# Kernel tuning notes

Hardware: AMD Instinct MI355X
Metric: run time of the kernel (lower is better)

The kernel has to match this reference:

```python
import jax, jax.numpy as jnp
import numpy as np

VOCAB = 90000
MAX_ID = 95000
EFFECT_DIM = 758
ADD_DIM = 10
EMBED_DIM = 768  # EFFECT_DIM + ADD_DIM
CTX = 1024
MAX_SYN = 8


def setup_inputs() -> dict:
    key = jax.random.key(0)
    k_ids, k_emb, k_rev, k_tab, k_msk = jax.random.split(key, 5)
    ids = jax.random.randint(k_ids, (CTX,), 0, VOCAB, dtype=jnp.int64)
    W_emb = jax.random.normal(k_emb, (MAX_ID, EFFECT_DIM), dtype=jnp.float32)
    W_rev = jax.random.normal(k_rev, (EMBED_DIM, MAX_ID), dtype=jnp.float32)
    padding = 0.1 * jnp.ones((CTX, ADD_DIM), dtype=jnp.float32)
    # synonym ids live in [VOCAB, MAX_ID); only some slots are active (variable-length lists)
    syn_table = jax.random.randint(k_tab, (MAX_ID, MAX_SYN), VOCAB, MAX_ID, dtype=jnp.int32)
    syn_mask = jax.random.randint(k_msk, (MAX_ID, MAX_SYN), 0, 2, dtype=jnp.int32)
    # tokens >= VOCAB (synonym ids themselves) have no synonyms
    syn_mask = syn_mask.at[VOCAB:].set(0)
    return {"ids": ids, "W_emb": W_emb, "W_rev": W_rev, "padding": padding,
            "syn_table": syn_table, "syn_mask": syn_mask}


def reference(ids, W_emb, W_rev, padding, syn_table, syn_mask):
    # VirtualEmbedding: base gather + masked synonym gather/scale/accumulate.
    # i_sum is computed BEFORE the synonym loop in the original, so each
    # synonym contribution is independent -> vectorized masked reduction.
    # (Dropout in eval mode is the identity.)
    base = W_emb[ids]                              # [L, D]
    syn_ids = syn_table[ids]                       # [L, K]
    syn = W_emb[syn_ids]                           # [L, K, D]
    mask = syn_mask[ids].astype(base.dtype)        # [L, K]
    i_sum = jnp.sum(base, axis=-1, keepdims=True)  # [L, 1]
    s_sum = jnp.sum(syn, axis=-1)                  # [L, K]
    d = i_sum / s_sum                              # [L, K]
    emb = base + jnp.einsum('lk,lkd->ld', mask * d, syn)
    # concat fixed context padding, then ReverseEmbedding projection to vocab
    full = jnp.concatenate([emb, padding], axis=1)  # [L, EMBED_DIM]
    return full @ W_rev                             # [L, MAX_ID]
```

## Files before the change

kernel.cpp:

```cpp
#include <hip/hip_runtime.h>
#include <stdint.h>

#define EFFECT_DIM 758
#define ADD_DIM 10
#define EMBED_DIM 768
#define NCOLS 95000
#define NSYN 8
#define NROWS 1024
#define NT256 372
#define TILE_B 32768

typedef __attribute__((ext_vector_type(8))) __bf16 bf16x8;
typedef __attribute__((ext_vector_type(16))) float f32x16;
typedef __attribute__((ext_vector_type(4))) uint32_t u32x4;


static __device__ __forceinline__ uint32_t pack2(float a, float b) {
  uint32_t r;
  asm("v_cvt_pk_bf16_f32 %0, %1, %2" : "=v"(r) : "v"(a), "v"(b));
  return r;
}

#define GLOAD16(src, dst)                                                   \
  __builtin_amdgcn_global_load_lds(                                         \
      (const __attribute__((address_space(1))) uint32_t*)(src),             \
      (__attribute__((address_space(3))) uint32_t*)(dst), 16, 0, 0)

#define F4C(f, i) ((i) == 0 ? (f).x : (i) == 1 ? (f).y : (i) == 2 ? (f).z : (f).w)

__global__ __launch_bounds__(256) void emb_kernel(
    const int* __restrict__ ids, const float* __restrict__ W_emb,
    const float* __restrict__ padding, const int* __restrict__ syn_table,
    const int* __restrict__ syn_mask, char* __restrict__ ws)
{
  const int l = blockIdx.x;
  const int t = threadIdx.x;
  const int id = ids[l];
  int sid[NSYN];
  int msk[NSYN];
#pragma unroll
  for (int k = 0; k < NSYN; ++k) {
    sid[k] = syn_table[id * NSYN + k];
    msk[k] = syn_mask[id * NSYN + k];
  }

  double p[9] = {0, 0, 0, 0, 0, 0, 0, 0, 0};
  for (int d = t; d < EFFECT_DIM; d += 256) {
    p[0] += (double)W_emb[(size_t)id * EFFECT_DIM + d];
#pragma unroll
    for (int k = 0; k < NSYN; ++k)
      p[k + 1] += (double)W_emb[(size_t)sid[k] * EFFECT_DIM + d];
  }

  __shared__ double s_red[9][4];
  const int w = t >> 6;
#pragma unroll
  for (int k = 0; k < 9; ++k) {
    double v = p[k];
#pragma unroll
    for (int off = 32; off > 0; off >>= 1) v += __shfl_down(v, off, 64);
    if ((t & 63) == 0) s_red[k][w] = v;
  }
  __syncthreads();

  const double isum = s_red[0][0] + s_red[0][1] + s_red[0][2] + s_red[0][3];
  float coef[NSYN];
#pragma unroll
  for (int k = 0; k < NSYN; ++k) {
    double ss = s_red[k + 1][0] + s_red[k + 1][1] + s_red[k + 1][2] + s_red[k + 1][3];
    coef[k] = msk[k] ? (float)(isum / ss) : 0.0f;
  }

  const int r = l & 255;
  char* wbase = ws + (size_t)(l >> 8) * (12 * TILE_B);

  for (int j = t; j < 384; j += 256) {
    const int d0 = 2 * j;
    float v0, v1;
    if (d0 < EFFECT_DIM) {
      const float* bp = W_emb + (size_t)id * EFFECT_DIM + d0;
      v0 = bp[0];
      v1 = bp[1];
#pragma unroll
      for (int k = 0; k < NSYN; ++k) {
        const float* sp = W_emb + (size_t)sid[k] * EFFECT_DIM + d0;
        v0 = fmaf(coef[k], sp[0], v0);
        v1 = fmaf(coef[k], sp[1], v1);
      }
    } else {
      v0 = padding[l * ADD_DIM + (d0 - EFFECT_DIM)];
      v1 = padding[l * ADD_DIM + (d0 + 1 - EFFECT_DIM)];
    }
    const int ks   = j >> 5;
    const int jl   = j & 31;
    const int kk   = jl >> 3;
    const int byte = (jl & 7) * 4;
    const int lane = (r & 31) + ((byte >> 4) << 5);
    *(uint32_t*)(wbase + ks * TILE_B + kk * 8192 + (r >> 5) * 1024 +
                 lane * 16 + (byte & 15)) = pack2(v0, v1);
  }
}

__global__ __launch_bounds__(256) void conv_kernel(
    const float* __restrict__ Wrev, char* __restrict__ Bbuf)
{
  __shared__ char lds[16384];
  const int t   = threadIdx.x;
  const int j   = blockIdx.x;
  const int ks  = blockIdx.y;
  const int nl4 = t & 31;
  const int kc  = t >> 5;
  const int gn4 = j * 128 + nl4 * 4;
  const bool valid = (gn4 + 4) <= NCOLS;

  float4 v[8];
  const float* p = Wrev + (size_t)(ks * 64 + kc * 8) * NCOLS + gn4;
#pragma unroll
  for (int jj = 0; jj < 8; ++jj)
    v[jj] = valid ? *(const float4*)(p + (size_t)jj * NCOLS)
                  : float4{0.0f, 0.0f, 0.0f, 0.0f};

  const int kk  = kc >> 1;
  const int lh2 = kc & 1;
#pragma unroll
  for (int i = 0; i < 4; ++i) {
    const int nloc = nl4 * 4 + i;
    u32x4 u;
#pragma unroll
    for (int j2 = 0; j2 < 4; ++j2)
      u[j2] = pack2(F4C(v[2 * j2], i), F4C(v[2 * j2 + 1], i));
    const int lane = (nloc & 31) + (lh2 << 5);
    *(u32x4*)(lds + kk * 4096 + (nl4 >> 3) * 1024 + lane * 16) = u;
  }
  __syncthreads();

  char* base = Bbuf + (size_t)((j >> 1) * 12 + ks) * TILE_B + (j & 1) * 4096;
#pragma unroll
  for (int i = 0; i < 4; ++i) {
    const int idx = i * 4096 + t * 16;
    const int k2  = idx >> 12;
    const int rem = idx & 4095;
    *(u32x4*)(base + k2 * 8192 + rem) = *(const u32x4*)(lds + idx);
  }
}

__global__ __launch_bounds__(512, 2) void gemm_pre(
    const char* __restrict__ Abuf, const char* __restrict__ Bbuf,
    float* __restrict__ out)
{
  extern __shared__ char lds[];
  const int t = threadIdx.x;
  const int l = t & 63;
  const int w = t >> 6;
  const int wm = w >> 2;
  const int wn = w & 3;

  const int wgid = blockIdx.x;
  const int xcd  = wgid & 7;
  const int work = xcd * 186 + (wgid >> 3);
  const int mt = work & 3;
  const int nt = work >> 2;
  const int n0 = nt * 256;

  const char* asrc = Abuf + (size_t)mt * (12 * TILE_B);
  const char* bsrc = Bbuf + (size_t)nt * (12 * TILE_B);
  const int soff = t * 16;
  const int doff = w * 1024;

#define STAGEU(s, ksi, kkk)                                                  \
  {                                                                          \
    GLOAD16(asrc + (ksi)*TILE_B + (kkk)*8192 + soff,                         \
            lds + (s)*65536 + (kkk)*8192 + doff);                            \
    GLOAD16(bsrc + (ksi)*TILE_B + (kkk)*8192 + soff,                         \
            lds + (s)*65536 + 32768 + (kkk)*8192 + doff);                    \
  }

#pragma unroll
  for (int kk = 0; kk < 4; ++kk) STAGEU(0, 0, kk);
  asm volatile("s_waitcnt vmcnt(0)" ::: "memory");
  __builtin_amdgcn_s_barrier();

  f32x16 acc[4][2] = {};

  for (int T = 0; T < 12; ++T) {
    const int cs = T & 1;
    const char* aw = lds + cs * 65536 + (wm * 4) * 1024 + l * 16;
    const char* bw = lds + cs * 65536 + 32768 + (wn * 2) * 1024 + l * 16;
    const bool pf = (T < 11);

#pragma unroll
    for (int p = 0; p < 4; ++p) {
      bf16x8 a[4], b[2];
#pragma unroll
      for (int mr = 0; mr < 4; ++mr)
        a[mr] = *(const bf16x8*)(aw + p * 8192 + mr * 1024);
#pragma unroll
      for (int nr = 0; nr < 2; ++nr)
        b[nr] = *(const bf16x8*)(bw + p * 8192 + nr * 1024);

      if (p == 0 && pf) {
#pragma unroll
        for (int u = 0; u < 4; ++u) STAGEU(cs ^ 1, T + 1, u);
      }
      __builtin_amdgcn_sched_barrier(0);
      __builtin_amdgcn_s_barrier();
      asm volatile("s_waitcnt lgkmcnt(0)" ::: "memory");
      __builtin_amdgcn_sched_barrier(0);

      __builtin_amdgcn_s_setprio(1);
#pragma unroll
      for (int mr = 0; mr < 4; ++mr)
#pragma unroll
        for (int nr = 0; nr < 2; ++nr)
          acc[mr][nr] = __builtin_amdgcn_mfma_f32_32x32x16_bf16(
              a[mr], b[nr], acc[mr][nr], 0, 0, 0);
      __builtin_amdgcn_s_setprio(0);
      __builtin_amdgcn_sched_barrier(0);

      if (p == 3 && pf)
        asm volatile("s_waitcnt vmcnt(0)" ::: "memory");
      __builtin_amdgcn_s_barrier();
    }
  }
#undef STAGEU

  const int lh = l >> 5;
#pragma unroll
  for (int nr = 0; nr < 2; ++nr) {
    const int gc = n0 + wn * 64 + nr * 32 + (l & 31);
    if (gc < NCOLS) {
#pragma unroll
      for (int mr = 0; mr < 4; ++mr)
#pragma unroll
        for (int reg = 0; reg < 16; ++reg) {
          const int row = mt * 256 + wm * 128 + mr * 32 +
                          (reg & 3) + 8 * (reg >> 2) + 4 * lh;
          __builtin_nontemporal_store(acc[mr][nr][reg],
                                      &out[(size_t)row * NCOLS + gc]);
        }
    }
  }
}

extern "C" void kernel_launch(void* const* d_in, const int* in_sizes, int n_in,
                              void* d_out, int out_size, void* d_ws, size_t ws_size,
                              hipStream_t stream) {
  const int*   ids       = (const int*)d_in[0];
  const float* W_emb     = (const float*)d_in[1];
  const float* W_rev     = (const float*)d_in[2];
  const float* padding   = (const float*)d_in[3];
  const int*   syn_table = (const int*)d_in[4];
  const int*   syn_mask  = (const int*)d_in[5];
  float* out = (float*)d_out;
  char*  ws  = (char*)d_ws;

  const size_t A_BYTES = (size_t)4 * 12 * TILE_B;

  hipLaunchKernelGGL(emb_kernel, dim3(NROWS), dim3(256), 0, stream,
                     ids, W_emb, padding, syn_table, syn_mask, ws);

  char* Bbuf = ws + A_BYTES;
  hipLaunchKernelGGL(conv_kernel, dim3(NT256 * 2, 12), dim3(256), 0, stream,
                     W_rev, Bbuf);

  hipLaunchKernelGGL(gemm_pre, dim3(4 * NT256), dim3(512), 131072, stream,
                     ws, Bbuf, out);
}
```

Before: 396.3 us.

## Use 4-wave GEMM workgroups with 128x128 wave tiles and register double-buffered fragments

New measurement: 399.9 us. No clear change (+0.9%).

```diff
diff --git a/kernel.cpp b/kernel.cpp
--- a/kernel.cpp
+++ b/kernel.cpp
@@ -144,7 +144,7 @@
   }
 }
 
-__global__ __launch_bounds__(512, 2) void gemm_pre(
+__global__ __launch_bounds__(256, 1) void gemm_pre(
     const char* __restrict__ Abuf, const char* __restrict__ Bbuf,
     float* __restrict__ out)
 {
@@ -152,8 +152,8 @@
   const int t = threadIdx.x;
   const int l = t & 63;
   const int w = t >> 6;
-  const int wm = w >> 2;
-  const int wn = w & 3;
+  const int wm = w >> 1;
+  const int wn = w & 1;
 
   const int wgid = blockIdx.x;
   const int xcd  = wgid & 7;
@@ -164,70 +164,73 @@
 
   const char* asrc = Abuf + (size_t)mt * (12 * TILE_B);
   const char* bsrc = Bbuf + (size_t)nt * (12 * TILE_B);
-  const int soff = t * 16;
-  const int doff = w * 1024;
-
-#define STAGEU(s, ksi, kkk)                                                  \
+
+#define STAGE(s, ksi)                                                        \
   {                                                                          \
-    GLOAD16(asrc + (ksi)*TILE_B + (kkk)*8192 + soff,                         \
-            lds + (s)*65536 + (kkk)*8192 + doff);                            \
-    GLOAD16(bsrc + (ksi)*TILE_B + (kkk)*8192 + soff,                         \
-            lds + (s)*65536 + 32768 + (kkk)*8192 + doff);                    \
-  }
-
-#pragma unroll
-  for (int kk = 0; kk < 4; ++kk) STAGEU(0, 0, kk);
+    _Pragma("unroll") for (int i = 0; i < 8; ++i) {                          \
+      GLOAD16(asrc + (ksi)*TILE_B + i*4096 + t*16,                           \
+              lds + (s)*65536 + i*4096 + w*1024);                            \
+      GLOAD16(bsrc + (ksi)*TILE_B + i*4096 + t*16,                           \
+              lds + (s)*65536 + 32768 + i*4096 + w*1024);                    \
+    }                                                                        \
+  }
+
+#define RDFRAGS(s, p, fa, fb)                                                \
+  {                                                                          \
+    const char* aw_ = lds + (s)*65536 + (p)*8192 + (wm*4)*1024 + l*16;       \
+    const char* bw_ = lds + (s)*65536 + 32768 + (p)*8192 + (wn*4)*1024 + l*16;\
+    _Pragma("unroll") for (int mr = 0; mr < 4; ++mr)                         \
+      fa[mr] = *(const bf16x8*)(aw_ + mr*1024);                              \
+    _Pragma("unroll") for (int nr = 0; nr < 4; ++nr)                         \
+      fb[nr] = *(const bf16x8*)(bw_ + nr*1024);                              \
+  }
+
+#define DOMFMA(fa, fb)                                                       \
+  {                                                                          \
+    __builtin_amdgcn_s_setprio(1);                                           \
+    _Pragma("unroll") for (int mr = 0; mr < 4; ++mr)                         \
+      _Pragma("unroll") for (int nr = 0; nr < 4; ++nr)                       \
+        acc[mr][nr] = __builtin_amdgcn_mfma_f32_32x32x16_bf16(               \
+            fa[mr], fb[nr], acc[mr][nr], 0, 0, 0);                           \
+    __builtin_amdgcn_s_setprio(0);                                           \
+  }
+
+  STAGE(0, 0);
   asm volatile("s_waitcnt vmcnt(0)" ::: "memory");
   __builtin_amdgcn_s_barrier();
 
-  f32x16 acc[4][2] = {};
+  bf16x8 fa0[4], fb0[4], fa1[4], fb1[4];
+  RDFRAGS(0, 0, fa0, fb0);
+
+  f32x16 acc[4][4] = {};
 
   for (int T = 0; T < 12; ++T) {
     const int cs = T & 1;
-    const char* aw = lds + cs * 65536 + (wm * 4) * 1024 + l * 16;
-    const char* bw = lds + cs * 65536 + 32768 + (wn * 2) * 1024 + l * 16;
     const bool pf = (T < 11);
 
-#pragma unroll
-    for (int p = 0; p < 4; ++p) {
-      bf16x8 a[4], b[2];
-#pragma unroll
-      for (int mr = 0; mr < 4; ++mr)
-        a[mr] = *(const bf16x8*)(aw + p * 8192 + mr * 1024);
-#pragma unroll
-      for (int nr = 0; nr < 2; ++nr)
-        b[nr] = *(const bf16x8*)(bw + p * 8192 + nr * 1024);
-
-      if (p == 0 && pf) {
-#pragma unroll
-        for (int u = 0; u < 4; ++u) STAGEU(cs ^ 1, T + 1, u);
-      }
+    RDFRAGS(cs, 1, fa1, fb1);
+    if (pf) STAGE(cs ^ 1, T + 1);
+    DOMFMA(fa0, fb0);
+    RDFRAGS(cs, 2, fa0, fb0);
+    DOMFMA(fa1, fb1);
+    RDFRAGS(cs, 3, fa1, fb1);
+    DOMFMA(fa0, fb0);
+    DOMFMA(fa1, fb1);
+    if (pf) {
+      asm volatile("s_waitcnt vmcnt(0)" ::: "memory");
       __builtin_amdgcn_sched_barrier(0);
       __builtin_amdgcn_s_barrier();
-      asm volatile("s_waitcnt lgkmcnt(0)" ::: "memory");
-      __builtin_amdgcn_sched_barrier(0);
-
-      __builtin_amdgcn_s_setprio(1);
-#pragma unroll
-      for (int mr = 0; mr < 4; ++mr)
-#pragma unroll
-        for (int nr = 0; nr < 2; ++nr)
-          acc[mr][nr] = __builtin_amdgcn_mfma_f32_32x32x16_bf16(
-              a[mr], b[nr], acc[mr][nr], 0, 0, 0);
-      __builtin_amdgcn_s_setprio(0);
-      __builtin_amdgcn_sched_barrier(0);
-
-      if (p == 3 && pf)
-        asm volatile("s_waitcnt vmcnt(0)" ::: "memory");
-      __builtin_amdgcn_s_barrier();
+      RDFRAGS(cs ^ 1, 0, fa0, fb0);
     }
   }
-#undef STAGEU
+#undef STAGE
+#undef RDFRAGS
+#undef DOMFMA
 
   const int lh = l >> 5;
 #pragma unroll
-  for (int nr = 0; nr < 2; ++nr) {
-    const int gc = n0 + wn * 64 + nr * 32 + (l & 31);
+  for (int nr = 0; nr < 4; ++nr) {
+    const int gc = n0 + wn * 128 + nr * 32 + (l & 31);
     if (gc < NCOLS) {
 #pragma unroll
       for (int mr = 0; mr < 4; ++mr)
@@ -263,6 +266,6 @@
   hipLaunchKernelGGL(conv_kernel, dim3(NT256 * 2, 12), dim3(256), 0, stream,
                      W_rev, Bbuf);
 
-  hipLaunchKernelGGL(gemm_pre, dim3(4 * NT256), dim3(512), 131072, stream,
+  hipLaunchKernelGGL(gemm_pre, dim3(4 * NT256), dim3(256), 131072, stream,
                      ws, Bbuf, out);
 }
```
